# Optimization experiments

Measured on AMD Instinct MI355X. Metric: run time of the kernel, lower is better.

The kernel has to match this reference:

```python
import jax, jax.numpy as jnp
import numpy as np

B, C, H, W = 4, 256, 64, 64
C8 = C // 8


def setup_inputs() -> dict:
    key = jax.random.key(0)
    ks = jax.random.split(key, 8)
    s = 1.0 / np.sqrt(C)
    return {
        "x_ccd": jax.random.normal(ks[0], (B, C, H, W), jnp.float32),
        "x_dem": jax.random.normal(ks[1], (B, C, H, W), jnp.float32),
        "Wq": jax.random.normal(ks[2], (C8, C), jnp.float32) * s,
        "bq": jax.random.normal(ks[3], (C8,), jnp.float32) * 0.01,
        "Wk": jax.random.normal(ks[4], (C8, C), jnp.float32) * s,
        "bk": jax.random.normal(ks[5], (C8,), jnp.float32) * 0.01,
        "Wv": jax.random.normal(ks[6], (C, C), jnp.float32) * s,
        "bv": jax.random.normal(ks[7], (C,), jnp.float32) * 0.01,
        "gamma": jnp.zeros((1,), jnp.float32),
    }


def reference(x_ccd, x_dem, Wq, bq, Wk, bk, Wv, bv, gamma):
    b, c, h, w = x_ccd.shape
    n = h * w
    xc = x_ccd.reshape(b, c, n)  # [B,C,N]
    xd = x_dem.reshape(b, c, n)
    # 1x1 convs == per-pixel linear projections
    q = jnp.einsum("oc,bcn->bno", Wq, xc) + bq  # [B,N,C8]
    k = jnp.einsum("oc,bcn->bon", Wk, xd) + bk[None, :, None]  # [B,C8,N]
    energy = jnp.einsum("bno,bom->bnm", q, k)  # [B,N,N]
    attention = jax.nn.softmax(energy, axis=-1)
    v = jnp.einsum("oc,bcn->bon", Wv, xd) + bv[None, :, None]  # [B,C,N]
    out = jnp.einsum("bom,bnm->bon", v, attention)  # value @ attention^T
    out = out.reshape(b, c, h, w)
    return gamma * out + x_ccd
```

## Files before the change

kernel.cpp:

```cpp
#include <hip/hip_runtime.h>

typedef unsigned short u16;
typedef unsigned int u32;
typedef short v8s __attribute__((ext_vector_type(8)));
typedef float v16f __attribute__((ext_vector_type(16)));
typedef unsigned int v2u __attribute__((ext_vector_type(2)));

#define MFMA(a, b, c) __builtin_amdgcn_mfma_f32_32x32x16_bf16(a, b, c, 0, 0, 0)
#define L2E 1.44269504088896f

union U8 { v8s s; uint4 u4; u32 u[4]; };

__device__ __forceinline__ u16 f2bf(float x) {
    u32 u = __float_as_uint(x);
    return (u16)((u + 0x7FFFu + ((u >> 16) & 1u)) >> 16);
}
__device__ __forceinline__ u32 pk2(float a, float b) {
    return (u32)f2bf(a) | ((u32)f2bf(b) << 16);
}
__device__ __forceinline__ u32 pkz(float e0, float e1) {
    return __builtin_amdgcn_perm(__float_as_uint(e1), __float_as_uint(e0), 0x07060302u);
}


__global__ __launch_bounds__(256) void prep_w_kernel(
    const float* __restrict__ Wq, const float* __restrict__ bq,
    const float* __restrict__ Wk, const float* __restrict__ bk,
    const float* __restrict__ Wv, const float* __restrict__ bv,
    u16* __restrict__ WfT, float* __restrict__ ball)
{
    int tid = blockIdx.x * 256 + threadIdx.x;
    if (tid < 81920) {
        int ch = tid >> 8, c = tid & 255;
        float w;
        if (ch < 32)      w = Wq[ch * 256 + c];
        else if (ch < 64) w = Wk[(ch - 32) * 256 + c] * L2E;
        else              w = Wv[(ch - 64) * 256 + c];
        int tile = (ch >> 5) * 16 + (c >> 4);
        int lane = ((c >> 3) & 1) * 32 + (ch & 31);
        WfT[tile * 512 + lane * 8 + (c & 7)] = f2bf(w);
    } else if (tid < 82240) {
        int i = tid - 81920;
        float bb;
        if (i < 32)      bb = bq[i];
        else if (i < 64) bb = bk[i - 32] * L2E;
        else             bb = bv[i - 64];
        ball[i] = bb;
    }
}

__global__ __launch_bounds__(256, 2) void proj_kernel(
    const float* __restrict__ xc, const float* __restrict__ xd,
    const u16* __restrict__ WfT, const float* __restrict__ ball,
    u16* __restrict__ qfT, u16* __restrict__ kfT, u16* __restrict__ vfT)
{
    __shared__ u16 xls[2][32][264];
    int blk = blockIdx.x, b = blk >> 7, n0 = (blk & 127) * 32;
    int t = threadIdx.x, lane = t & 63, wv = t >> 6;
    int hl = lane >> 5, l31 = lane & 31;

#pragma unroll
    for (int p = 0; p < 4; p++) {
        int s = p * 256 + t;
        int arr = s >> 9, c4 = (s >> 3) & 63, n4s = s & 7;
        const float* src = arr ? xd : xc;
        size_t g0 = ((size_t)(b * 256 + c4 * 4)) * 4096 + n0 + n4s * 4;
        float4 r0 = *(const float4*)&src[g0];
        float4 r1 = *(const float4*)&src[g0 + 4096];
        float4 r2 = *(const float4*)&src[g0 + 8192];
        float4 r3 = *(const float4*)&src[g0 + 12288];
        *(uint2*)&xls[arr][n4s * 4 + 0][c4 * 4] = make_uint2(pk2(r0.x, r1.x), pk2(r2.x, r3.x));
        *(uint2*)&xls[arr][n4s * 4 + 1][c4 * 4] = make_uint2(pk2(r0.y, r1.y), pk2(r2.y, r3.y));
        *(uint2*)&xls[arr][n4s * 4 + 2][c4 * 4] = make_uint2(pk2(r0.z, r1.z), pk2(r2.z, r3.z));
        *(uint2*)&xls[arr][n4s * 4 + 3][c4 * 4] = make_uint2(pk2(r0.w, r1.w), pk2(r2.w, r3.w));
    }
    __syncthreads();

    int jobs[3];
    int nj;
    if (wv == 0)      { jobs[0] = 0; jobs[1] = 2; jobs[2] = 0; nj = 2; }
    else if (wv == 1) { jobs[0] = 1; jobs[1] = 3; jobs[2] = 0; nj = 2; }
    else if (wv == 2) { jobs[0] = 4; jobs[1] = 5; jobs[2] = 6; nj = 3; }
    else              { jobs[0] = 7; jobs[1] = 8; jobs[2] = 9; nj = 3; }

    int nt = blk & 127;
    int n = n0 + l31;
    int vl = ((n >> 3) & 1) * 32, tk = n >> 4, j8 = n & 7;

    for (int jj = 0; jj < nj; jj++) {
        int j = jobs[jj];
        int arr = (j != 0);
        const u16* wb = WfT + (size_t)(j * 16) * 512 + lane * 8;
        v16f acc = {};
#pragma unroll
        for (int kc = 0; kc < 16; kc++) {
            U8 bx, a;
            bx.u4 = *(const uint4*)&xls[arr][l31][kc * 16 + hl * 8];
            a.u4  = *(const uint4*)(wb + (size_t)kc * 512);
            acc = MFMA(a.s, bx.s, acc);
        }
        if (j <= 1) {
            u16* dst = j ? kfT : qfT;
#pragma unroll
            for (int i = 0; i < 8; i++) {
                int r = 2 * i;
                int row = (r & 3) + 8 * (r >> 2) + 4 * hl;
                float b0 = ball[j * 32 + row], b1 = ball[j * 32 + row + 1];
                u32 st = pk2(acc[r] + b0, acc[r + 1] + b1);
                size_t off = (((size_t)(b * 128 + nt) * 2 + (row >> 4)) * 512)
                           + (((row >> 3) & 1) * 32 + l31) * 8 + (row & 7);
                *(u32*)&dst[off] = st;
            }
        } else {
            int vi = j - 2;
            u16* vdst = vfT + (((size_t)(b * 8 + vi) * 256 + tk) * 512) + vl * 8 + j8;
#pragma unroll
            for (int r = 0; r < 16; r++) {
                int row = (r & 3) + 8 * (r >> 2) + 4 * hl;
                vdst[row * 8] = f2bf(acc[r] + ball[64 + vi * 32 + row]);
            }
        }
    }
}

__global__ __launch_bounds__(512, 2) void flash_kernel(
    const u16* __restrict__ qfT, const u16* __restrict__ kfT,
    const u16* __restrict__ vfT, const float* __restrict__ xccd,
    const float* __restrict__ gptr, float* __restrict__ outp)
{
    __shared__ float red[2][2][4][16][64];
    __shared__ float lred[2][2][32];

    const int t = threadIdx.x, lane = t & 63, wv = t >> 6;
    const int hl = lane >> 5, l31 = lane & 31;
    const int blk = blockIdx.x;
    const int b = (blk & 7) >> 1;
    const int qt = ((blk >> 3) << 1) | (blk & 1);
    const int kh = wv & 1, chh = (wv >> 1) & 1, qh = wv >> 2;
    const int n0 = qt * 64 + qh * 32;
    const int chbase = chh * 128;

    U8 qf0, qf1;
    {
        const u16* qp = qfT + ((size_t)(b * 128 + (n0 >> 5)) * 2) * 512 + lane * 8;
        qf0.u4 = *(const uint4*)qp;
        qf1.u4 = *(const uint4*)(qp + 512);
    }
    U8 ones;
#pragma unroll
    for (int i = 0; i < 8; i++) ones.s[i] = (short)0x3F80;

    v16f acc[4] = {};
    v16f lac = {};

    const u16* kbase = kfT + ((size_t)b * 128 * 2) * 512 + lane * 8;
    const u16* vbase = vfT + ((size_t)(b * 8 + chh * 4) * 256) * 512 + lane * 8;

    U8 k0[2], k1[2], k2[2], v0[4][2], v1[4][2], v2[4][2];

    auto load_frags = [&](int it, U8 (&kf)[2], U8 (&vf)[4][2]) {
        const int kt = it * 2 + kh;
        kf[0].u4 = *(const uint4*)(kbase + (size_t)(kt * 2) * 512);
        kf[1].u4 = *(const uint4*)(kbase + (size_t)(kt * 2 + 1) * 512);
        const int tk = it * 4 + kh * 2;
#pragma unroll
        for (int ct = 0; ct < 4; ct++) {
            const u16* vp = vbase + ((size_t)(ct * 256 + tk)) * 512;
            vf[ct][0].u4 = *(const uint4*)vp;
            vf[ct][1].u4 = *(const uint4*)(vp + 512);
        }
    };

    load_frags(0, k0, v0);
    load_frags(1, k1, v1);

    v16f Ecur;
    {
        v16f E = {};
        E = MFMA(k0[0].s, qf0.s, E);
        E = MFMA(k0[1].s, qf1.s, E);
        Ecur = E;
    }

    auto step = [&](int it, U8 (&kf)[2], U8 (&vf)[4][2], U8 (&kn)[2], U8 (&vn)[4][2],
                    U8 (&knx)[2], bool doqk) {
        if (it + 2 < 64) load_frags(it + 2, kn, vn);

        u32 pkv[8];
#pragma unroll
        for (int j = 0; j < 8; j++)
            pkv[j] = pkz(__builtin_amdgcn_exp2f(Ecur[2 * j]),
                         __builtin_amdgcn_exp2f(Ecur[2 * j + 1]));
        U8 B0, B1;
        {
            v2u r;
            r = __builtin_amdgcn_permlane32_swap(pkv[0], pkv[2], 0, 0); B0.u[0] = r[0]; B0.u[2] = r[1];
            r = __builtin_amdgcn_permlane32_swap(pkv[1], pkv[3], 0, 0); B0.u[1] = r[0]; B0.u[3] = r[1];
            r = __builtin_amdgcn_permlane32_swap(pkv[4], pkv[6], 0, 0); B1.u[0] = r[0]; B1.u[2] = r[1];
            r = __builtin_amdgcn_permlane32_swap(pkv[5], pkv[7], 0, 0); B1.u[1] = r[0]; B1.u[3] = r[1];
        }

        __builtin_amdgcn_s_setprio(1);
        if (doqk) {
            v16f E = {};
            E = MFMA(knx[0].s, qf0.s, E);
            E = MFMA(knx[1].s, qf1.s, E);
            Ecur = E;
        }
        if (chh == 0) {
            lac = MFMA(ones.s, B0.s, lac);
            lac = MFMA(ones.s, B1.s, lac);
        }
#pragma unroll
        for (int ct = 0; ct < 4; ct++) {
            acc[ct] = MFMA(vf[ct][0].s, B0.s, acc[ct]);
            acc[ct] = MFMA(vf[ct][1].s, B1.s, acc[ct]);
        }
        __builtin_amdgcn_s_setprio(0);
    };

#pragma unroll 1
    for (int base = 0; base < 63; base += 3) {
        step(base,     k0, v0, k2, v2, k1, true);
        step(base + 1, k1, v1, k0, v0, k2, true);
        step(base + 2, k2, v2, k1, v1, k0, true);
    }
    step(63, k0, v0, k1, v1, k1, false);

    if (chh == 0 && lane < 32) lred[qh][kh][l31] = lac[0];
    if (kh == 1) {
#pragma unroll
        for (int ct = 0; ct < 4; ct++)
#pragma unroll
            for (int r = 0; r < 16; r++)
                red[qh][chh][ct][r][lane] = acc[ct][r];
    }
    __syncthreads();
    if (kh == 0) {
        const float g = gptr[0];
        const float sc = g / (lred[qh][0][l31] + lred[qh][1][l31]);
#pragma unroll
        for (int ct = 0; ct < 4; ct++)
#pragma unroll
            for (int r = 0; r < 16; r++) {
                float v = acc[ct][r] + red[qh][chh][ct][r][lane];
                int ch = chbase + ct * 32 + (r & 3) + 8 * (r >> 2) + 4 * hl;
                size_t ga = ((size_t)(b * 256 + ch)) * 4096 + n0 + l31;
                outp[ga] = v * sc + xccd[ga];
            }
    }
}

extern "C" void kernel_launch(void* const* d_in, const int* in_sizes, int n_in,
                              void* d_out, int out_size, void* d_ws, size_t ws_size,
                              hipStream_t stream)
{
    const float* xc    = (const float*)d_in[0];
    const float* xd    = (const float*)d_in[1];
    const float* Wq    = (const float*)d_in[2];
    const float* bq    = (const float*)d_in[3];
    const float* Wk    = (const float*)d_in[4];
    const float* bk    = (const float*)d_in[5];
    const float* Wv    = (const float*)d_in[6];
    const float* bv    = (const float*)d_in[7];
    const float* gamma = (const float*)d_in[8];
    float* out = (float*)d_out;

    u16* qfT  = (u16*)d_ws;
    u16* kfT  = qfT + (size_t)524288;
    u16* vfT  = kfT + (size_t)524288;
    u16* WfT  = vfT + (size_t)4194304;
    float* bl = (float*)(WfT + 81920);

    prep_w_kernel<<<322, 256, 0, stream>>>(Wq, bq, Wk, bk, Wv, bv, WfT, bl);
    proj_kernel<<<512, 256, 0, stream>>>(xc, xd, WfT, bl, qfT, kfT, vfT);
    flash_kernel<<<256, 512, 0, stream>>>(qfT, kfT, vfT, xc, gamma, out);
}
```

Before: 162.9 us.

## Split flash work into 32-query blocks with 64-channel waves and VALU row sums

The flash kernel now handles one 32-query tile per block across 512 blocks. Each wave covers 64 output channels instead of 128, which shrinks per-wave accumulators and fragment buffers so launch bounds can target 4 blocks per CU. The softmax row-sum moves from an MFMA against a ones vector to a VALU sum of the bf16-rounded exponentials. The software pipeline is simplified to double buffering, with QK computed in-step rather than one step ahead. In exchange, each block re-reads all K/V for only 32 queries, which doubles global K/V traffic, and there is less overlap between the QK MFMA and the exp work.

```diff
diff --git a/kernel.cpp b/kernel.cpp
--- a/kernel.cpp
+++ b/kernel.cpp
@@ -123,74 +123,66 @@
     }
 }
 
-__global__ __launch_bounds__(512, 2) void flash_kernel(
+__global__ __launch_bounds__(512, 4) void flash_kernel(
     const u16* __restrict__ qfT, const u16* __restrict__ kfT,
     const u16* __restrict__ vfT, const float* __restrict__ xccd,
     const float* __restrict__ gptr, float* __restrict__ outp)
 {
-    __shared__ float red[2][2][4][16][64];
-    __shared__ float lred[2][2][32];
+    __shared__ float red[4][2][16][64];
+    __shared__ float lred[2][32];
 
     const int t = threadIdx.x, lane = t & 63, wv = t >> 6;
     const int hl = lane >> 5, l31 = lane & 31;
     const int blk = blockIdx.x;
     const int b = (blk & 7) >> 1;
     const int qt = ((blk >> 3) << 1) | (blk & 1);
-    const int kh = wv & 1, chh = (wv >> 1) & 1, qh = wv >> 2;
-    const int n0 = qt * 64 + qh * 32;
-    const int chbase = chh * 128;
+    const int kh = wv & 1, chq = wv >> 1;
+    const int n0 = qt * 32;
 
     U8 qf0, qf1;
     {
-        const u16* qp = qfT + ((size_t)(b * 128 + (n0 >> 5)) * 2) * 512 + lane * 8;
+        const u16* qp = qfT + ((size_t)(b * 128 + qt) * 2) * 512 + lane * 8;
         qf0.u4 = *(const uint4*)qp;
         qf1.u4 = *(const uint4*)(qp + 512);
     }
-    U8 ones;
-#pragma unroll
-    for (int i = 0; i < 8; i++) ones.s[i] = (short)0x3F80;
-
-    v16f acc[4] = {};
-    v16f lac = {};
-
-    const u16* kbase = kfT + ((size_t)b * 128 * 2) * 512 + lane * 8;
-    const u16* vbase = vfT + ((size_t)(b * 8 + chh * 4) * 256) * 512 + lane * 8;
-
-    U8 k0[2], k1[2], k2[2], v0[4][2], v1[4][2], v2[4][2];
-
-    auto load_frags = [&](int it, U8 (&kf)[2], U8 (&vf)[4][2]) {
-        const int kt = it * 2 + kh;
-        kf[0].u4 = *(const uint4*)(kbase + (size_t)(kt * 2) * 512);
-        kf[1].u4 = *(const uint4*)(kbase + (size_t)(kt * 2 + 1) * 512);
-        const int tk = it * 4 + kh * 2;
-#pragma unroll
-        for (int ct = 0; ct < 4; ct++) {
-            const u16* vp = vbase + ((size_t)(ct * 256 + tk)) * 512;
-            vf[ct][0].u4 = *(const uint4*)vp;
-            vf[ct][1].u4 = *(const uint4*)(vp + 512);
-        }
+
+    v16f acc[2] = {};
+    float lrun = 0.f;
+
+    const u16* kp = kfT + ((size_t)(b * 128 + kh)) * 1024 + lane * 8;
+    const u16* vp = vfT + (((size_t)(b * 8 + chq * 2) * 256) + 2 * kh) * 512 + lane * 8;
+
+    U8 k0[2], k1[2], v0[2][2], v1[2][2];
+
+    auto load_frags = [&](U8 (&kf)[2], U8 (&vf)[2][2], int it) {
+        const u16* k = kp + (size_t)it * 2048;
+        kf[0].u4 = *(const uint4*)k;
+        kf[1].u4 = *(const uint4*)(k + 512);
+        const u16* v = vp + (size_t)it * 2048;
+        vf[0][0].u4 = *(const uint4*)v;
+        vf[0][1].u4 = *(const uint4*)(v + 512);
+        vf[1][0].u4 = *(const uint4*)(v + 131072);
+        vf[1][1].u4 = *(const uint4*)(v + 131072 + 512);
     };
 
-    load_frags(0, k0, v0);
-    load_frags(1, k1, v1);
-
-    v16f Ecur;
-    {
+    auto step = [&](U8 (&kf)[2], U8 (&vf)[2][2]) {
         v16f E = {};
-        E = MFMA(k0[0].s, qf0.s, E);
-        E = MFMA(k0[1].s, qf1.s, E);
-        Ecur = E;
-    }
-
-    auto step = [&](int it, U8 (&kf)[2], U8 (&vf)[4][2], U8 (&kn)[2], U8 (&vn)[4][2],
-                    U8 (&knx)[2], bool doqk) {
-        if (it + 2 < 64) load_frags(it + 2, kn, vn);
-
+        E = MFMA(kf[0].s, qf0.s, E);
+        E = MFMA(kf[1].s, qf1.s, E);
         u32 pkv[8];
 #pragma unroll
         for (int j = 0; j < 8; j++)
-            pkv[j] = pkz(__builtin_amdgcn_exp2f(Ecur[2 * j]),
-                         __builtin_amdgcn_exp2f(Ecur[2 * j + 1]));
+            pkv[j] = pkz(__builtin_amdgcn_exp2f(E[2 * j]),
+                         __builtin_amdgcn_exp2f(E[2 * j + 1]));
+        if (chq == 0) {
+            float sl = 0.f;
+#pragma unroll
+            for (int j = 0; j < 8; j++) {
+                sl += __uint_as_float(pkv[j] & 0xFFFF0000u);
+                sl += __uint_as_float(pkv[j] << 16);
+            }
+            lrun += sl;
+        }
         U8 B0, B1;
         {
             v2u r;
@@ -199,52 +191,46 @@
             r = __builtin_amdgcn_permlane32_swap(pkv[4], pkv[6], 0, 0); B1.u[0] = r[0]; B1.u[2] = r[1];
             r = __builtin_amdgcn_permlane32_swap(pkv[5], pkv[7], 0, 0); B1.u[1] = r[0]; B1.u[3] = r[1];
         }
-
         __builtin_amdgcn_s_setprio(1);
-        if (doqk) {
-            v16f E = {};
-            E = MFMA(knx[0].s, qf0.s, E);
-            E = MFMA(knx[1].s, qf1.s, E);
-            Ecur = E;
-        }
-        if (chh == 0) {
-            lac = MFMA(ones.s, B0.s, lac);
-            lac = MFMA(ones.s, B1.s, lac);
-        }
-#pragma unroll
-        for (int ct = 0; ct < 4; ct++) {
-            acc[ct] = MFMA(vf[ct][0].s, B0.s, acc[ct]);
-            acc[ct] = MFMA(vf[ct][1].s, B1.s, acc[ct]);
-        }
+        acc[0] = MFMA(vf[0][0].s, B0.s, acc[0]);
+        acc[0] = MFMA(vf[0][1].s, B1.s, acc[0]);
+        acc[1] = MFMA(vf[1][0].s, B0.s, acc[1]);
+        acc[1] = MFMA(vf[1][1].s, B1.s, acc[1]);
         __builtin_amdgcn_s_setprio(0);
     };
 
+    load_frags(k0, v0, 0);
 #pragma unroll 1
-    for (int base = 0; base < 63; base += 3) {
-        step(base,     k0, v0, k2, v2, k1, true);
-        step(base + 1, k1, v1, k0, v0, k2, true);
-        step(base + 2, k2, v2, k1, v1, k0, true);
-    }
-    step(63, k0, v0, k1, v1, k1, false);
-
-    if (chh == 0 && lane < 32) lred[qh][kh][l31] = lac[0];
+    for (int it = 0; it < 64; it += 2) {
+        load_frags(k1, v1, it + 1);
+        step(k0, v0);
+        if (it + 2 < 64) load_frags(k0, v0, it + 2);
+        step(k1, v1);
+    }
+
     if (kh == 1) {
 #pragma unroll
-        for (int ct = 0; ct < 4; ct++)
+        for (int ct = 0; ct < 2; ct++)
 #pragma unroll
             for (int r = 0; r < 16; r++)
-                red[qh][chh][ct][r][lane] = acc[ct][r];
+                red[chq][ct][r][lane] = acc[ct][r];
+    }
+    if (chq == 0) {
+        v2u rr = __builtin_amdgcn_permlane32_swap(__float_as_uint(lrun),
+                                                  __float_as_uint(lrun), 0, 0);
+        float ltot = __uint_as_float(rr[0]) + __uint_as_float(rr[1]);
+        if (lane < 32) lred[kh][l31] = ltot;
     }
     __syncthreads();
     if (kh == 0) {
         const float g = gptr[0];
-        const float sc = g / (lred[qh][0][l31] + lred[qh][1][l31]);
-#pragma unroll
-        for (int ct = 0; ct < 4; ct++)
+        const float sc = g / (lred[0][l31] + lred[1][l31]);
+#pragma unroll
+        for (int ct = 0; ct < 2; ct++)
 #pragma unroll
             for (int r = 0; r < 16; r++) {
-                float v = acc[ct][r] + red[qh][chh][ct][r][lane];
-                int ch = chbase + ct * 32 + (r & 3) + 8 * (r >> 2) + 4 * hl;
+                float v = acc[ct][r] + red[chq][ct][r][lane];
+                int ch = chq * 64 + ct * 32 + (r & 3) + 8 * (r >> 2) + 4 * hl;
                 size_t ga = ((size_t)(b * 256 + ch)) * 4096 + n0 + l31;
                 outp[ga] = v * sc + xccd[ga];
             }
@@ -274,5 +260,5 @@
 
     prep_w_kernel<<<322, 256, 0, stream>>>(Wq, bq, Wk, bk, Wv, bv, WfT, bl);
     proj_kernel<<<512, 256, 0, stream>>>(xc, xd, WfT, bl, qfT, kfT, vfT);
-    flash_kernel<<<256, 512, 0, stream>>>(qfT, kfT, vfT, xc, gamma, out);
-}
+    flash_kernel<<<512, 512, 0, stream>>>(qfT, kfT, vfT, xc, gamma, out);
+}
```

New measurement: 173.1 us. 6.2% more time.
